# Kernel tuning notes

Hardware: AMD Instinct MI355X
Metric: run time of the kernel (lower is better)

Reference implementation:

```python
import jax, jax.numpy as jnp
import numpy as np

N_NODES = 100000
N_EDGES = 2000000
F_IN = 64
HID = 64
N_MP = 6  # hidden message-passing layers


def setup_inputs() -> dict:
    key = jax.random.key(0)
    ks = jax.random.split(key, 8)
    x = jax.random.normal(ks[0], (N_NODES, F_IN), dtype=jnp.float32)
    edge_index = jax.random.randint(ks[1], (2, N_EDGES), 0, N_NODES, dtype=jnp.int64)
    # GCNConv params: weight [in, out], bias [out] (glorot-ish scale)
    def w(k, i, o):
        return jax.random.normal(k, (i, o), dtype=jnp.float32) * (1.0 / np.sqrt(i))
    W_i = w(ks[2], F_IN, HID)
    b_i = jnp.zeros((HID,), jnp.float32)
    W_h = jax.random.normal(ks[3], (N_MP, HID, HID), dtype=jnp.float32) * (1.0 / np.sqrt(HID))
    b_h = jnp.zeros((N_MP, HID), jnp.float32)
    W_o = w(ks[4], HID, 1)
    b_o = jnp.zeros((1,), jnp.float32)
    return {"x": x, "edge_index": edge_index, "W_i": W_i, "b_i": b_i,
            "W_h": W_h, "b_h": b_h, "W_o": W_o, "b_o": b_o}


def reference(x, edge_index, W_i, b_i, W_h, b_h, W_o, b_o):
    n = x.shape[0]
    loop = jnp.arange(n, dtype=edge_index.dtype)
    # add self loops (PyG GCNConv default)
    src = jnp.concatenate([edge_index[0], loop])  # [E+N]
    dst = jnp.concatenate([edge_index[1], loop])
    # symmetric normalization: deg computed over dst (col) with self loops
    deg = jax.ops.segment_sum(jnp.ones(dst.shape, x.dtype), dst, num_segments=n)
    dinv = jax.lax.rsqrt(deg)  # deg >= 1 due to self loops
    norm = (dinv[src] * dinv[dst])[:, None]  # [E+N, 1]

    def conv(h, W, b):
        h = h @ W                                   # [N, out]
        msg = h[src] * norm                         # gather + scale  [E+N, out]
        return jax.ops.segment_sum(msg, dst, num_segments=n) + b

    h = jax.nn.relu(conv(x, W_i, b_i))
    for l in range(W_h.shape[0]):
        h = jax.nn.relu(conv(h, W_h[l], b_h[l]))
    return conv(h, W_o, b_o)  # [N, 1]
```

## Files before the change

### kernel.cpp

```cpp
#include <hip/hip_runtime.h>
#include <math.h>

#define TPB 256
#define BSH 8
#define BMAX 512
#define EPB 4096


__global__ __launch_bounds__(TPB) void k_hist(const int* __restrict__ dst,
                                              int* __restrict__ bucketCnt,
                                              int nE, int nbuck) {
  __shared__ int h[BMAX];
  for (int i = threadIdx.x; i < BMAX; i += TPB) h[i] = 0;
  __syncthreads();
  int base = blockIdx.x * EPB;
  for (int i = threadIdx.x; i < EPB; i += TPB) {
    int e = base + i;
    if (e < nE) atomicAdd(&h[dst[e] >> BSH], 1);
  }
  __syncthreads();
  for (int i = threadIdx.x; i < nbuck; i += TPB)
    if (h[i]) atomicAdd(&bucketCnt[i], h[i]);
}

__global__ __launch_bounds__(BMAX) void k_bscan(const int* __restrict__ bucketCnt,
                                                int* __restrict__ bOff,
                                                int* __restrict__ gCur,
                                                int* __restrict__ rowPtr,
                                                int nbuck, int n, int nE) {
  __shared__ int sd[BMAX];
  int t = threadIdx.x;
  int v = (t < nbuck) ? bucketCnt[t] : 0;
  sd[t] = v;
  __syncthreads();
  for (int off = 1; off < BMAX; off <<= 1) {
    int add = (t >= off) ? sd[t - off] : 0;
    __syncthreads();
    sd[t] += add;
    __syncthreads();
  }
  if (t < nbuck) {
    bOff[t + 1] = sd[t];
    gCur[t] = sd[t] - v;
  }
  if (t == 0) { bOff[0] = 0; rowPtr[n] = nE; }
}

__global__ __launch_bounds__(TPB) void k_bucket(const int* __restrict__ src,
                                                const int* __restrict__ dst,
                                                int* __restrict__ gCur,
                                                int* __restrict__ pairBuf,
                                                int nE, int nbuck) {
  __shared__ int   hist[BMAX];
  __shared__ int   baseL[BMAX];
  __shared__ int   sp[EPB];
  __shared__ short sbk[EPB];
  for (int i = threadIdx.x; i < BMAX; i += TPB) hist[i] = 0;
  __syncthreads();
  int cb = blockIdx.x * EPB;
  for (int i = threadIdx.x; i < EPB; i += TPB) {
    int e = cb + i;
    if (e < nE) {
      int s = src[e], d = dst[e];
      int b = d >> BSH;
      sp[i]  = s | ((d & ((1 << BSH) - 1)) << 20);
      sbk[i] = (short)b;
      atomicAdd(&hist[b], 1);
    } else sbk[i] = -1;
  }
  __syncthreads();
  for (int i = threadIdx.x; i < nbuck; i += TPB)
    baseL[i] = hist[i] ? atomicAdd(&gCur[i], hist[i]) : 0;
  __syncthreads();
  for (int i = threadIdx.x; i < BMAX; i += TPB) hist[i] = 0;
  __syncthreads();
  for (int i = threadIdx.x; i < EPB; i += TPB) {
    int b = sbk[i];
    if (b >= 0) {
      int r = atomicAdd(&hist[b], 1);
      pairBuf[baseL[b] + r] = sp[i];
    }
  }
}

__global__ __launch_bounds__(TPB) void k_final(const int* __restrict__ pairBuf,
                                               const int* __restrict__ bOff,
                                               int* __restrict__ rowPtr,
                                               int* __restrict__ col,
                                               float* __restrict__ dinv,
                                               int n) {
  __shared__ int h[TPB];
  __shared__ int ex[TPB];
  int t = threadIdx.x;
  int b = blockIdx.x;
  int p0 = bOff[b], p1 = bOff[b + 1];
  h[t] = 0;
  __syncthreads();
  for (int i = p0 + t; i < p1; i += TPB)
    atomicAdd(&h[pairBuf[i] >> 20], 1);
  __syncthreads();
  int v = h[t];
  ex[t] = v;
  __syncthreads();
  for (int off = 1; off < TPB; off <<= 1) {
    int add = (t >= off) ? ex[t - off] : 0;
    __syncthreads();
    ex[t] += add;
    __syncthreads();
  }
  int excl = ex[t] - v;
  int node = (b << BSH) + t;
  if (node < n) {
    rowPtr[node] = p0 + excl;
    dinv[node]   = rsqrtf((float)(v + 1));
  }
  __syncthreads();
  h[t] = excl;
  __syncthreads();
  for (int i = p0 + t; i < p1; i += TPB) {
    int p = pairBuf[i];
    int r = atomicAdd(&h[p >> 20], 1);
    col[p0 + r] = p & 0xFFFFF;
  }
}


__global__ __launch_bounds__(TPB, 4) void k_gemm(const float* __restrict__ H,
                                                 const float* __restrict__ W,
                                                 const float* __restrict__ dinv,
                                                 float* __restrict__ HWS,
                                                 int relu, int rows) {
  __shared__ float Wl[64 * 64];
  __shared__ float Hl[64][68];
  const int tid = threadIdx.x;
  const int c0 = (tid & 15) * 4;
  const int r0 = (tid >> 4) * 4;
  const int row0 = blockIdx.x * 64;

  for (int i = tid; i < 64 * 16; i += TPB)
    ((float4*)Wl)[i] = ((const float4*)W)[i];

  for (int i = tid; i < 64 * 16; i += TPB) {
    int r = i >> 4, q = i & 15;
    int gr = row0 + r;
    float4 v = make_float4(0.f, 0.f, 0.f, 0.f);
    if (gr < rows) v = ((const float4*)(H + (size_t)gr * 64))[q];
    if (relu) {
      v.x = fmaxf(v.x, 0.f); v.y = fmaxf(v.y, 0.f);
      v.z = fmaxf(v.z, 0.f); v.w = fmaxf(v.w, 0.f);
    }
    *(float4*)&Hl[r][q * 4] = v;
  }
  __syncthreads();

  float acc[4][4] = {{0.f,0.f,0.f,0.f},{0.f,0.f,0.f,0.f},
                     {0.f,0.f,0.f,0.f},{0.f,0.f,0.f,0.f}};
#pragma unroll 4
  for (int k = 0; k < 64; ++k) {
    float4 w = *(const float4*)&Wl[k * 64 + c0];
    float h0 = Hl[r0 + 0][k];
    float h1 = Hl[r0 + 1][k];
    float h2 = Hl[r0 + 2][k];
    float h3 = Hl[r0 + 3][k];
    acc[0][0] = fmaf(h0, w.x, acc[0][0]); acc[0][1] = fmaf(h0, w.y, acc[0][1]);
    acc[0][2] = fmaf(h0, w.z, acc[0][2]); acc[0][3] = fmaf(h0, w.w, acc[0][3]);
    acc[1][0] = fmaf(h1, w.x, acc[1][0]); acc[1][1] = fmaf(h1, w.y, acc[1][1]);
    acc[1][2] = fmaf(h1, w.z, acc[1][2]); acc[1][3] = fmaf(h1, w.w, acc[1][3]);
    acc[2][0] = fmaf(h2, w.x, acc[2][0]); acc[2][1] = fmaf(h2, w.y, acc[2][1]);
    acc[2][2] = fmaf(h2, w.z, acc[2][2]); acc[2][3] = fmaf(h2, w.w, acc[2][3]);
    acc[3][0] = fmaf(h3, w.x, acc[3][0]); acc[3][1] = fmaf(h3, w.y, acc[3][1]);
    acc[3][2] = fmaf(h3, w.z, acc[3][2]); acc[3][3] = fmaf(h3, w.w, acc[3][3]);
  }

#pragma unroll
  for (int i = 0; i < 4; ++i) {
    int gr = row0 + r0 + i;
    if (gr < rows) {
      float s = dinv[gr];
      float4 o = make_float4(acc[i][0] * s, acc[i][1] * s,
                             acc[i][2] * s, acc[i][3] * s);
      *(float4*)&HWS[(size_t)gr * 64 + c0] = o;
    }
  }
}

__global__ __launch_bounds__(TPB) void k_scatter(const float* __restrict__ HWS,
                                                 const int* __restrict__ rowPtr,
                                                 const int* __restrict__ col,
                                                 const float* __restrict__ dinv,
                                                 const float* __restrict__ bias,
                                                 float* __restrict__ OUT, int n) {
  int wave = blockIdx.x * (TPB / 64) + (threadIdx.x >> 6);
  if (wave >= n) return;
  const int lane = threadIdx.x & 63;
  const int eg = lane >> 4;
  const int q  = lane & 15;
  const int node = wave;

  float4 acc = make_float4(0.f, 0.f, 0.f, 0.f);
  if (eg == 0)
    acc = *(const float4*)&HWS[(size_t)node * 64 + q * 4];

  const int e0 = rowPtr[node];
  const int deg = rowPtr[node + 1] - e0;

  for (int base = 0; base < deg; base += 64) {
    int m = deg - base; if (m > 64) m = 64;
    int idxv = (lane < m) ? col[e0 + base + lane] : 0;
    int j = 0;
    for (; j + 16 <= m; j += 16) {
      int s0 = __shfl(idxv, j + eg,      64);
      int s1 = __shfl(idxv, j + 4 + eg,  64);
      int s2 = __shfl(idxv, j + 8 + eg,  64);
      int s3 = __shfl(idxv, j + 12 + eg, 64);
      float4 v0 = *(const float4*)&HWS[(size_t)s0 * 64 + q * 4];
      float4 v1 = *(const float4*)&HWS[(size_t)s1 * 64 + q * 4];
      float4 v2 = *(const float4*)&HWS[(size_t)s2 * 64 + q * 4];
      float4 v3 = *(const float4*)&HWS[(size_t)s3 * 64 + q * 4];
      acc.x += (v0.x + v1.x) + (v2.x + v3.x);
      acc.y += (v0.y + v1.y) + (v2.y + v3.y);
      acc.z += (v0.z + v1.z) + (v2.z + v3.z);
      acc.w += (v0.w + v1.w) + (v2.w + v3.w);
    }
    for (; j + 8 <= m; j += 8) {
      int s0 = __shfl(idxv, j + eg,     64);
      int s1 = __shfl(idxv, j + 4 + eg, 64);
      float4 v0 = *(const float4*)&HWS[(size_t)s0 * 64 + q * 4];
      float4 v1 = *(const float4*)&HWS[(size_t)s1 * 64 + q * 4];
      acc.x += v0.x + v1.x;
      acc.y += v0.y + v1.y;
      acc.z += v0.z + v1.z;
      acc.w += v0.w + v1.w;
    }
    for (; j < m; j += 4) {
      int jj = j + eg;
      int jc = (jj < m) ? jj : (m - 1);
      int s = __shfl(idxv, jc, 64);
      if (jj < m) {
        float4 v = *(const float4*)&HWS[(size_t)s * 64 + q * 4];
        acc.x += v.x; acc.y += v.y; acc.z += v.z; acc.w += v.w;
      }
    }
  }

#pragma unroll
  for (int off = 16; off < 64; off <<= 1) {
    acc.x += __shfl_xor(acc.x, off, 64);
    acc.y += __shfl_xor(acc.y, off, 64);
    acc.z += __shfl_xor(acc.z, off, 64);
    acc.w += __shfl_xor(acc.w, off, 64);
  }

  if (eg == 0) {
    float s = dinv[node];
    float4 b4 = *(const float4*)&bias[q * 4];
    float4 o = make_float4(acc.x * s + b4.x, acc.y * s + b4.y,
                           acc.z * s + b4.z, acc.w * s + b4.w);
    *(float4*)&OUT[(size_t)node * 64 + q * 4] = o;
  }
}

__global__ __launch_bounds__(TPB) void k_fdot(const float* __restrict__ H,
                                              const float* __restrict__ Wo,
                                              const float* __restrict__ dinv,
                                              float* __restrict__ hws1, int n) {
  int i = blockIdx.x * TPB + threadIdx.x;
  if (i >= n) return;
  const float4* Hv = (const float4*)(H + (size_t)i * 64);
  float acc = 0.f;
#pragma unroll
  for (int q = 0; q < 16; ++q) {
    float4 v = Hv[q];
    acc += fmaxf(v.x, 0.f) * Wo[4 * q + 0];
    acc += fmaxf(v.y, 0.f) * Wo[4 * q + 1];
    acc += fmaxf(v.z, 0.f) * Wo[4 * q + 2];
    acc += fmaxf(v.w, 0.f) * Wo[4 * q + 3];
  }
  hws1[i] = acc * dinv[i];
}

__global__ __launch_bounds__(TPB) void k_fscat(const float* __restrict__ hws1,
                                               const int* __restrict__ rowPtr,
                                               const int* __restrict__ col,
                                               const float* __restrict__ dinv,
                                               const float* __restrict__ bo,
                                               float* __restrict__ out, int n) {
  int i = blockIdx.x * TPB + threadIdx.x;
  if (i >= n) return;
  float a0 = hws1[i], a1 = 0.f, a2 = 0.f, a3 = 0.f;
  int e0 = rowPtr[i], e1 = rowPtr[i + 1];
  int e = e0;
  for (; e + 4 <= e1; e += 4) {
    a0 += hws1[col[e]];
    a1 += hws1[col[e + 1]];
    a2 += hws1[col[e + 2]];
    a3 += hws1[col[e + 3]];
  }
  for (; e < e1; ++e) a0 += hws1[col[e]];
  out[i] = dinv[i] * ((a0 + a1) + (a2 + a3)) + bo[0];
}


extern "C" void kernel_launch(void* const* d_in, const int* in_sizes, int n_in,
                              void* d_out, int out_size, void* d_ws, size_t ws_size,
                              hipStream_t stream) {
  const float* x   = (const float*)d_in[0];
  const int*   ei  = (const int*)d_in[1];
  const float* W_i = (const float*)d_in[2];
  const float* b_i = (const float*)d_in[3];
  const float* W_h = (const float*)d_in[4];
  const float* b_h = (const float*)d_in[5];
  const float* W_o = (const float*)d_in[6];
  const float* b_o = (const float*)d_in[7];

  const int N = in_sizes[0] / 64;
  const int E = in_sizes[1] / 2;
  const int* srcArr = ei;
  const int* dstArr = ei + E;
  const int nbuck = (N + (1 << BSH) - 1) >> BSH;

  char* w = (char*)d_ws;
  auto take = [&](size_t bytes) -> char* {
    char* p = w;
    w += (bytes + 255) & ~(size_t)255;
    return p;
  };
  int*   rowPtr    = (int*)take((size_t)(N + 1) * 4);
  int*   col       = (int*)take((size_t)E * 4);
  float* dinv      = (float*)take((size_t)N * 4);
  int*   bucketCnt = (int*)take((size_t)BMAX * 4);
  int*   bOff      = (int*)take((size_t)(BMAX + 1) * 4);
  int*   gCur      = (int*)take((size_t)BMAX * 4);
  float* bufH      = (float*)take((size_t)N * 64 * 4);
  float* bufS      = (float*)take((size_t)N * 64 * 4);
  float* hws1      = (float*)take((size_t)N * 4);
  int*   pairBuf   = (int*)bufS;
  (void)ws_size; (void)n_in; (void)out_size;

  const int nbN    = (N + TPB - 1) / TPB;
  const int nbEd   = (E + EPB - 1) / EPB;
  const int nbGemm = (N + 63) / 64;
  const int nbScat = (N + 3) / 4;

  hipMemsetAsync(bucketCnt, 0, (size_t)BMAX * 4, stream);
  k_hist  <<<nbEd, TPB, 0, stream>>>(dstArr, bucketCnt, E, nbuck);
  k_bscan <<<1, BMAX, 0, stream>>>(bucketCnt, bOff, gCur, rowPtr, nbuck, N, E);
  k_bucket<<<nbEd, TPB, 0, stream>>>(srcArr, dstArr, gCur, pairBuf, E, nbuck);
  k_final <<<nbuck, TPB, 0, stream>>>(pairBuf, bOff, rowPtr, col, dinv, N);

  k_gemm   <<<nbGemm, TPB, 0, stream>>>(x, W_i, dinv, bufS, 0, N);
  k_scatter<<<nbScat, TPB, 0, stream>>>(bufS, rowPtr, col, dinv, b_i, bufH, N);

  for (int l = 0; l < 6; ++l) {
    k_gemm   <<<nbGemm, TPB, 0, stream>>>(bufH, W_h + (size_t)l * 64 * 64, dinv, bufS, 1, N);
    k_scatter<<<nbScat, TPB, 0, stream>>>(bufS, rowPtr, col, dinv, b_h + (size_t)l * 64, bufH, N);
  }

  k_fdot <<<nbN, TPB, 0, stream>>>(bufH, W_o, dinv, hws1, N);
  k_fscat<<<nbN, TPB, 0, stream>>>(hws1, rowPtr, col, dinv, b_o, (float*)d_out, N);
}
```

Baseline: 713.3 us.

## Split feature tables into four 16-column slices for cache-local gathers

```diff
diff --git a/kernel.cpp b/kernel.cpp
--- a/kernel.cpp
+++ b/kernel.cpp
@@ -129,7 +129,8 @@
                                                  const float* __restrict__ W,
                                                  const float* __restrict__ dinv,
                                                  float* __restrict__ HWS,
-                                                 int relu, int rows) {
+                                                 int relu, int denseIn,
+                                                 int rows, int N16) {
   __shared__ float Wl[64 * 64];
   __shared__ float Hl[64][68];
   const int tid = threadIdx.x;
@@ -140,16 +141,32 @@
   for (int i = tid; i < 64 * 16; i += TPB)
     ((float4*)Wl)[i] = ((const float4*)W)[i];
 
-  for (int i = tid; i < 64 * 16; i += TPB) {
-    int r = i >> 4, q = i & 15;
-    int gr = row0 + r;
-    float4 v = make_float4(0.f, 0.f, 0.f, 0.f);
-    if (gr < rows) v = ((const float4*)(H + (size_t)gr * 64))[q];
-    if (relu) {
-      v.x = fmaxf(v.x, 0.f); v.y = fmaxf(v.y, 0.f);
-      v.z = fmaxf(v.z, 0.f); v.w = fmaxf(v.w, 0.f);
-    }
-    *(float4*)&Hl[r][q * 4] = v;
+  if (denseIn) {
+    for (int i = tid; i < 64 * 16; i += TPB) {
+      int r = i >> 4, q = i & 15;
+      int gr = row0 + r;
+      float4 v = make_float4(0.f, 0.f, 0.f, 0.f);
+      if (gr < rows) v = ((const float4*)(H + (size_t)gr * 64))[q];
+      if (relu) {
+        v.x = fmaxf(v.x, 0.f); v.y = fmaxf(v.y, 0.f);
+        v.z = fmaxf(v.z, 0.f); v.w = fmaxf(v.w, 0.f);
+      }
+      *(float4*)&Hl[r][q * 4] = v;
+    }
+  } else {
+    for (int i = tid; i < 64 * 16; i += TPB) {
+      int r = i >> 4, q = i & 15;
+      int sl = q >> 2, off = (q & 3) * 4;
+      int gr = row0 + r;
+      float4 v = make_float4(0.f, 0.f, 0.f, 0.f);
+      if (gr < rows)
+        v = *(const float4*)&H[(size_t)sl * N16 + (size_t)gr * 16 + off];
+      if (relu) {
+        v.x = fmaxf(v.x, 0.f); v.y = fmaxf(v.y, 0.f);
+        v.z = fmaxf(v.z, 0.f); v.w = fmaxf(v.w, 0.f);
+      }
+      *(float4*)&Hl[r][q * 4] = v;
+    }
   }
   __syncthreads();
 
@@ -172,6 +189,8 @@
     acc[3][2] = fmaf(h3, w.z, acc[3][2]); acc[3][3] = fmaf(h3, w.w, acc[3][3]);
   }
 
+  const int sOut = c0 >> 4;
+  const int coff = c0 & 15;
 #pragma unroll
   for (int i = 0; i < 4; ++i) {
     int gr = row0 + r0 + i;
@@ -179,27 +198,31 @@
       float s = dinv[gr];
       float4 o = make_float4(acc[i][0] * s, acc[i][1] * s,
                              acc[i][2] * s, acc[i][3] * s);
-      *(float4*)&HWS[(size_t)gr * 64 + c0] = o;
-    }
-  }
-}
-
-__global__ __launch_bounds__(TPB) void k_scatter(const float* __restrict__ HWS,
-                                                 const int* __restrict__ rowPtr,
-                                                 const int* __restrict__ col,
-                                                 const float* __restrict__ dinv,
-                                                 const float* __restrict__ bias,
-                                                 float* __restrict__ OUT, int n) {
-  int wave = blockIdx.x * (TPB / 64) + (threadIdx.x >> 6);
-  if (wave >= n) return;
+      *(float4*)&HWS[(size_t)sOut * N16 + (size_t)gr * 16 + coff] = o;
+    }
+  }
+}
+
+__global__ __launch_bounds__(TPB) void k_scat4(const float* __restrict__ HWS,
+                                               const int* __restrict__ rowPtr,
+                                               const int* __restrict__ col,
+                                               const float* __restrict__ dinv,
+                                               const float* __restrict__ bias,
+                                               float* __restrict__ OUT,
+                                               int n, int N16) {
+  const int slice = blockIdx.x & 3;
+  const int nb    = blockIdx.x >> 2;
+  const int wv    = threadIdx.x >> 6;
+  const int node  = nb * 4 + wv;
+  if (node >= n) return;
   const int lane = threadIdx.x & 63;
-  const int eg = lane >> 4;
-  const int q  = lane & 15;
-  const int node = wave;
+  const int es = lane >> 2;
+  const int q  = lane & 3;
+  const float* __restrict__ tab = HWS + (size_t)slice * N16;
 
   float4 acc = make_float4(0.f, 0.f, 0.f, 0.f);
-  if (eg == 0)
-    acc = *(const float4*)&HWS[(size_t)node * 64 + q * 4];
+  if (es == 0)
+    acc = *(const float4*)&tab[(size_t)node * 16 + q * 4];
 
   const int e0 = rowPtr[node];
   const int deg = rowPtr[node + 1] - e0;
@@ -209,72 +232,56 @@
     int idxv = (lane < m) ? col[e0 + base + lane] : 0;
     int j = 0;
     for (; j + 16 <= m; j += 16) {
-      int s0 = __shfl(idxv, j + eg,      64);
-      int s1 = __shfl(idxv, j + 4 + eg,  64);
-      int s2 = __shfl(idxv, j + 8 + eg,  64);
-      int s3 = __shfl(idxv, j + 12 + eg, 64);
-      float4 v0 = *(const float4*)&HWS[(size_t)s0 * 64 + q * 4];
-      float4 v1 = *(const float4*)&HWS[(size_t)s1 * 64 + q * 4];
-      float4 v2 = *(const float4*)&HWS[(size_t)s2 * 64 + q * 4];
-      float4 v3 = *(const float4*)&HWS[(size_t)s3 * 64 + q * 4];
-      acc.x += (v0.x + v1.x) + (v2.x + v3.x);
-      acc.y += (v0.y + v1.y) + (v2.y + v3.y);
-      acc.z += (v0.z + v1.z) + (v2.z + v3.z);
-      acc.w += (v0.w + v1.w) + (v2.w + v3.w);
-    }
-    for (; j + 8 <= m; j += 8) {
-      int s0 = __shfl(idxv, j + eg,     64);
-      int s1 = __shfl(idxv, j + 4 + eg, 64);
-      float4 v0 = *(const float4*)&HWS[(size_t)s0 * 64 + q * 4];
-      float4 v1 = *(const float4*)&HWS[(size_t)s1 * 64 + q * 4];
-      acc.x += v0.x + v1.x;
-      acc.y += v0.y + v1.y;
-      acc.z += v0.z + v1.z;
-      acc.w += v0.w + v1.w;
-    }
-    for (; j < m; j += 4) {
-      int jj = j + eg;
+      int s = __shfl(idxv, j + es, 64);
+      float4 v = *(const float4*)&tab[(size_t)s * 16 + q * 4];
+      acc.x += v.x; acc.y += v.y; acc.z += v.z; acc.w += v.w;
+    }
+    for (; j < m; j += 16) {
+      int jj = j + es;
       int jc = (jj < m) ? jj : (m - 1);
       int s = __shfl(idxv, jc, 64);
       if (jj < m) {
-        float4 v = *(const float4*)&HWS[(size_t)s * 64 + q * 4];
+        float4 v = *(const float4*)&tab[(size_t)s * 16 + q * 4];
         acc.x += v.x; acc.y += v.y; acc.z += v.z; acc.w += v.w;
       }
     }
   }
 
 #pragma unroll
-  for (int off = 16; off < 64; off <<= 1) {
+  for (int off = 4; off < 64; off <<= 1) {
     acc.x += __shfl_xor(acc.x, off, 64);
     acc.y += __shfl_xor(acc.y, off, 64);
     acc.z += __shfl_xor(acc.z, off, 64);
     acc.w += __shfl_xor(acc.w, off, 64);
   }
 
-  if (eg == 0) {
+  if (es == 0) {
     float s = dinv[node];
-    float4 b4 = *(const float4*)&bias[q * 4];
+    float4 b4 = *(const float4*)&bias[slice * 16 + q * 4];
     float4 o = make_float4(acc.x * s + b4.x, acc.y * s + b4.y,
                            acc.z * s + b4.z, acc.w * s + b4.w);
-    *(float4*)&OUT[(size_t)node * 64 + q * 4] = o;
+    *(float4*)&OUT[(size_t)slice * N16 + (size_t)node * 16 + q * 4] = o;
   }
 }
 
 __global__ __launch_bounds__(TPB) void k_fdot(const float* __restrict__ H,
                                               const float* __restrict__ Wo,
                                               const float* __restrict__ dinv,
-                                              float* __restrict__ hws1, int n) {
+                                              float* __restrict__ hws1,
+                                              int n, int N16) {
   int i = blockIdx.x * TPB + threadIdx.x;
   if (i >= n) return;
-  const float4* Hv = (const float4*)(H + (size_t)i * 64);
   float acc = 0.f;
 #pragma unroll
-  for (int q = 0; q < 16; ++q) {
-    float4 v = Hv[q];
-    acc += fmaxf(v.x, 0.f) * Wo[4 * q + 0];
-    acc += fmaxf(v.y, 0.f) * Wo[4 * q + 1];
-    acc += fmaxf(v.z, 0.f) * Wo[4 * q + 2];
-    acc += fmaxf(v.w, 0.f) * Wo[4 * q + 3];
+  for (int s = 0; s < 4; ++s) {
+#pragma unroll
+    for (int t = 0; t < 4; ++t) {
+      float4 v = *(const float4*)&H[(size_t)s * N16 + (size_t)i * 16 + t * 4];
+      acc += fmaxf(v.x, 0.f) * Wo[s * 16 + t * 4 + 0];
+      acc += fmaxf(v.y, 0.f) * Wo[s * 16 + t * 4 + 1];
+      acc += fmaxf(v.z, 0.f) * Wo[s * 16 + t * 4 + 2];
+      acc += fmaxf(v.w, 0.f) * Wo[s * 16 + t * 4 + 3];
+    }
   }
   hws1[i] = acc * dinv[i];
 }
@@ -315,6 +322,7 @@
 
   const int N = in_sizes[0] / 64;
   const int E = in_sizes[1] / 2;
+  const int N16 = N * 16;
   const int* srcArr = ei;
   const int* dstArr = ei + E;
   const int nbuck = (N + (1 << BSH) - 1) >> BSH;
@@ -340,7 +348,7 @@
   const int nbN    = (N + TPB - 1) / TPB;
   const int nbEd   = (E + EPB - 1) / EPB;
   const int nbGemm = (N + 63) / 64;
-  const int nbScat = (N + 3) / 4;
+  const int nbScat = 4 * ((N + 3) / 4);
 
   hipMemsetAsync(bucketCnt, 0, (size_t)BMAX * 4, stream);
   k_hist  <<<nbEd, TPB, 0, stream>>>(dstArr, bucketCnt, E, nbuck);
@@ -348,14 +356,14 @@
   k_bucket<<<nbEd, TPB, 0, stream>>>(srcArr, dstArr, gCur, pairBuf, E, nbuck);
   k_final <<<nbuck, TPB, 0, stream>>>(pairBuf, bOff, rowPtr, col, dinv, N);
 
-  k_gemm   <<<nbGemm, TPB, 0, stream>>>(x, W_i, dinv, bufS, 0, N);
-  k_scatter<<<nbScat, TPB, 0, stream>>>(bufS, rowPtr, col, dinv, b_i, bufH, N);
+  k_gemm <<<nbGemm, TPB, 0, stream>>>(x, W_i, dinv, bufS, 0, 1, N, N16);
+  k_scat4<<<nbScat, TPB, 0, stream>>>(bufS, rowPtr, col, dinv, b_i, bufH, N, N16);
 
   for (int l = 0; l < 6; ++l) {
-    k_gemm   <<<nbGemm, TPB, 0, stream>>>(bufH, W_h + (size_t)l * 64 * 64, dinv, bufS, 1, N);
-    k_scatter<<<nbScat, TPB, 0, stream>>>(bufS, rowPtr, col, dinv, b_h + (size_t)l * 64, bufH, N);
-  }
-
-  k_fdot <<<nbN, TPB, 0, stream>>>(bufH, W_o, dinv, hws1, N);
+    k_gemm <<<nbGemm, TPB, 0, stream>>>(bufH, W_h + (size_t)l * 64 * 64, dinv, bufS, 1, 0, N, N16);
+    k_scat4<<<nbScat, TPB, 0, stream>>>(bufS, rowPtr, col, dinv, b_h + (size_t)l * 64, bufH, N, N16);
+  }
+
+  k_fdot <<<nbN, TPB, 0, stream>>>(bufH, W_o, dinv, hws1, N, N16);
   k_fscat<<<nbN, TPB, 0, stream>>>(hws1, rowPtr, col, dinv, b_o, (float*)d_out, N);
 }
```

After: 1.130 ms. 58.5% more time.
